# Kernel tuning notes

Measured on AMD Instinct MI355X. Metric: run time of the kernel, lower is better.

## Reference

```python
import jax, jax.numpy as jnp
import numpy as np

N_NODES = 100000
D = 128          # out_channels
H = 128          # hidden_dim
N_EDGES = 1000000


def setup_inputs() -> dict:
    key = jax.random.key(0)
    k_z, k_e, k_w1, k_b1, k_w2, k_b2 = jax.random.split(key, 6)
    z = jax.random.normal(k_z, (N_NODES, D), dtype=jnp.float32)
    edge_label_index = jax.random.randint(k_e, (2, N_EDGES), 0, N_NODES, dtype=jnp.int64)
    # nn.Linear default init: U(-1/sqrt(fan_in), 1/sqrt(fan_in))
    lim1 = 1.0 / np.sqrt(2 * D)
    lim2 = 1.0 / np.sqrt(H)
    W1 = jax.random.uniform(k_w1, (2 * D, H), jnp.float32, -lim1, lim1)
    b1 = jax.random.uniform(k_b1, (H,), jnp.float32, -lim1, lim1)
    W2 = jax.random.uniform(k_w2, (H, 1), jnp.float32, -lim2, lim2)
    b2 = jax.random.uniform(k_b2, (1,), jnp.float32, -lim2, lim2)
    return {"z": z, "edge_label_index": edge_label_index,
            "W1": W1, "b1": b1, "W2": W2, "b2": b2}


def reference(z, edge_label_index, W1, b1, W2, b2):
    src = edge_label_index[0]
    dst = edge_label_index[1]
    # gather + concat -> [n_edges, 2D]
    edge_feat = jnp.concatenate([z[src], z[dst]], axis=-1)
    h = jax.nn.relu(edge_feat @ W1 + b1)        # [n_edges, H]
    out = (h @ W2 + b2).squeeze(-1)             # [n_edges]
    return out
```

## Files before the change

kernel.cpp:

```cpp
#include <hip/hip_runtime.h>
#include <hip/hip_fp16.h>

typedef _Float16 half_t;
typedef __attribute__((ext_vector_type(2))) _Float16 f16x2;
typedef __attribute__((ext_vector_type(8))) _Float16 f16x8;
typedef __attribute__((ext_vector_type(4))) float f32x4;


__global__ void prep_kernel(const float* __restrict__ z,
                            const float* __restrict__ W1,
                            half_t* __restrict__ zh,
                            half_t* __restrict__ w1s, int n8) {
    if (blockIdx.x < 128) {
        const int t = blockIdx.x * 256 + threadIdx.x;
        const int j  = t & 7;
        const int L  = (t >> 3) & 63;
        const int nt = (t >> 9) & 15;
        const int ks = t >> 13;
        const int k    = ks * 32 + (L >> 4) * 8 + j;
        const int ncol = nt * 16 + (L & 15);
        const int row  = (ncol < 128) ? k : 128 + k;
        w1s[t] = (half_t)W1[row * 128 + (ncol & 127)];
    } else {
        const int t = (blockIdx.x - 128) * 256 + threadIdx.x;
        if (t < n8) {
            const float4 a = reinterpret_cast<const float4*>(z)[2 * t];
            const float4 b = reinterpret_cast<const float4*>(z)[2 * t + 1];
            f16x8 o;
            o[0] = (_Float16)a.x; o[1] = (_Float16)a.y;
            o[2] = (_Float16)a.z; o[3] = (_Float16)a.w;
            o[4] = (_Float16)b.x; o[5] = (_Float16)b.y;
            o[6] = (_Float16)b.z; o[7] = (_Float16)b.w;
            reinterpret_cast<f16x8*>(zh)[t] = o;
        }
    }
}

__global__ __launch_bounds__(256, 2)
void gemm_uv_kernel(const half_t* __restrict__ zh,
                    const half_t* __restrict__ w1s,
                    half_t* __restrict__ Y,
                    int n_groups, int stride_groups) {
    __shared__ __align__(16) half_t w1_lds[32768];
    const int wave = threadIdx.x >> 6;
    const int lane = threadIdx.x & 63;

#pragma unroll
    for (int rnd = 0; rnd < 16; ++rnd) {
        const int chunk = rnd * 4 + wave;
        const char* gp = (const char*)w1s + chunk * 1024 + lane * 16;
        __builtin_amdgcn_global_load_lds(
            (const __attribute__((address_space(1))) void*)gp,
            (__attribute__((address_space(3))) void*)
                ((char*)w1_lds + chunk * 1024),
            16, 0, 0);
    }
    __syncthreads();

    const int nlo  = lane & 15;
    const int quad = lane >> 4;
    const f16x8* blds = reinterpret_cast<const f16x8*>(w1_lds);

    int g = blockIdx.x * 4 + wave;
    if (g >= n_groups) return;

    const half_t* arow = zh + ((size_t)(g * 16 + nlo) * 128) + quad * 8;
    f16x8 av[4];
#pragma unroll
    for (int ks = 0; ks < 4; ++ks)
        av[ks] = *reinterpret_cast<const f16x8*>(arow + ks * 32);

    for (; g < n_groups; g += stride_groups) {
        const int gn = g + stride_groups;
        const int gp = (gn < n_groups) ? gn : g;
        const half_t* arow_n = zh + ((size_t)(gp * 16 + nlo) * 128) + quad * 8;
        f16x8 avn[4];
#pragma unroll
        for (int ks = 0; ks < 4; ++ks)
            avn[ks] = *reinterpret_cast<const f16x8*>(arow_n + ks * 32);

        f32x4 acc[16];
#pragma unroll
        for (int nt = 0; nt < 16; ++nt) acc[nt] = (f32x4){0.f, 0.f, 0.f, 0.f};

#pragma unroll
        for (int ks = 0; ks < 4; ++ks) {
            const f16x8* bp = blds + ks * 1024 + lane;
#pragma unroll
            for (int nt = 0; nt < 16; ++nt)
                acc[nt] = __builtin_amdgcn_mfma_f32_16x16x32_f16(
                    av[ks], bp[nt * 64], acc[nt], 0, 0, 0);
        }

#pragma unroll
        for (int r = 0; r < 4; ++r) {
            const int nr = g * 16 + quad * 4 + r;
            f16x8 up, vp;
#pragma unroll
            for (int t = 0; t < 8; ++t) {
                up[t] = (_Float16)acc[t][r];
                vp[t] = (_Float16)acc[8 + t][r];
            }
            *reinterpret_cast<f16x8*>(Y + (size_t)nr * 256 + nlo * 8) = up;
            *reinterpret_cast<f16x8*>(Y + (size_t)nr * 256 + 128 + nlo * 8) = vp;
        }

#pragma unroll
        for (int ks = 0; ks < 4; ++ks) av[ks] = avn[ks];
    }
}

static __device__ __forceinline__ f16x2 pair2(const f16x8& v, int p) {
    f16x2 r; r[0] = v[2 * p]; r[1] = v[2 * p + 1]; return r;
}

__global__ __launch_bounds__(256, 8)
void edge_decode_kernel(const half_t* __restrict__ Y,
                        const int* __restrict__ eidx,
                        const float* __restrict__ b1,
                        const float* __restrict__ W2,
                        const float* __restrict__ b2,
                        float* __restrict__ out,
                        int n_edges, int stride_e) {
    __shared__ __align__(16) half_t b1h[128];
    __shared__ __align__(16) half_t w2h[128];
    if (threadIdx.x < 128) {
        const int i = threadIdx.x;
        const int n = (i & 7) * 16 + (i >> 3);
        b1h[i] = (half_t)b1[n];
        w2h[i] = (half_t)W2[n];
    }
    __syncthreads();

    const int lane  = threadIdx.x & 63;
    const int sl    = lane & 15;
    const int eslot = lane >> 4;
    const f16x8 bv = reinterpret_cast<const f16x8*>(b1h)[sl];
    const f16x8 wv = reinterpret_cast<const f16x8*>(w2h)[sl];
    const float b2v = b2[0];
    const f16x2 zero2 = {(_Float16)0, (_Float16)0};

    const int w = blockIdx.x * 4 + (threadIdx.x >> 6);
    int e0 = w * 4;
    if (e0 >= n_edges) return;

    int ec = e0 + eslot; if (ec >= n_edges) ec = 0;
    int s1 = eidx[ec];
    int d1 = eidx[n_edges + ec];
    f16x8 u0 = *reinterpret_cast<const f16x8*>(Y + (size_t)s1 * 256 + sl * 8);
    f16x8 v0 = *reinterpret_cast<const f16x8*>(Y + (size_t)d1 * 256 + 128 +
                                               sl * 8);
    {
        int en = e0 + stride_e + eslot;
        if (en >= n_edges) en = 0;
        s1 = eidx[en];
        d1 = eidx[n_edges + en];
    }

    for (; e0 < n_edges; e0 += stride_e) {
        const int e = e0 + eslot;
        const bool valid = (e < n_edges);

        const f16x8 u1 = *reinterpret_cast<const f16x8*>(
            Y + (size_t)s1 * 256 + sl * 8);
        const f16x8 v1 = *reinterpret_cast<const f16x8*>(
            Y + (size_t)d1 * 256 + 128 + sl * 8);

        {
            int en = e0 + 2 * stride_e + eslot;
            if (en >= n_edges) en = 0;
            s1 = eidx[en];
            d1 = eidx[n_edges + en];
        }

        float acc = 0.f;
#pragma unroll
        for (int p = 0; p < 4; ++p) {
            f16x2 h2 = pair2(u0, p) + pair2(v0, p) + pair2(bv, p);
            h2 = __builtin_elementwise_max(h2, zero2);
            acc = __builtin_amdgcn_fdot2(h2, pair2(wv, p), acc, false);
        }
        acc += __shfl_xor(acc, 1);
        acc += __shfl_xor(acc, 2);
        acc += __shfl_xor(acc, 4);
        acc += __shfl_xor(acc, 8);
        if (sl == 0 && valid) out[e] = acc + b2v;

        u0 = u1; v0 = v1;
    }
}

__global__ void naive_edge_kernel(const float* __restrict__ z,
                                  const int* __restrict__ eidx,
                                  const float* __restrict__ W1,
                                  const float* __restrict__ b1,
                                  const float* __restrict__ W2,
                                  const float* __restrict__ b2,
                                  float* __restrict__ out, int n_edges) {
    __shared__ float feat[256];
    __shared__ float red[2];
    const int e = blockIdx.x;
    const int t = threadIdx.x;
    const int s = eidx[e], d = eidx[n_edges + e];
    feat[t] = z[(size_t)s * 128 + t];
    feat[128 + t] = z[(size_t)d * 128 + t];
    __syncthreads();
    float h = b1[t];
    for (int k = 0; k < 256; ++k) h = fmaf(feat[k], W1[k * 128 + t], h);
    float p = fmaxf(h, 0.f) * W2[t];
    for (int off = 32; off; off >>= 1) p += __shfl_down(p, off);
    if ((t & 63) == 0) red[t >> 6] = p;
    __syncthreads();
    if (t == 0) out[e] = red[0] + red[1] + b2[0];
}

extern "C" void kernel_launch(void* const* d_in, const int* in_sizes, int n_in,
                              void* d_out, int out_size, void* d_ws,
                              size_t ws_size, hipStream_t stream) {
    const float* z   = (const float*)d_in[0];
    const int* eidx  = (const int*)d_in[1];
    const float* W1  = (const float*)d_in[2];
    const float* b1  = (const float*)d_in[3];
    const float* W2  = (const float*)d_in[4];
    const float* b2  = (const float*)d_in[5];
    float* out       = (float*)d_out;

    const int nz      = in_sizes[0];
    const int n_nodes = nz / 128;
    const int n_edges = in_sizes[1] / 2;

    const size_t Y_bytes   = (size_t)n_nodes * 256 * sizeof(half_t);
    const size_t zh_bytes  = (size_t)nz * sizeof(half_t);
    const size_t w1s_bytes = 32768 * sizeof(half_t);

    if (ws_size >= Y_bytes + zh_bytes + w1s_bytes) {
        half_t* Y   = (half_t*)d_ws;
        half_t* zh  = (half_t*)((char*)d_ws + Y_bytes);
        half_t* w1s = (half_t*)((char*)d_ws + Y_bytes + zh_bytes);

        const int n8 = nz / 8;
        const int zblocks = (n8 + 255) / 256;
        prep_kernel<<<128 + zblocks, 256, 0, stream>>>(z, W1, zh, w1s, n8);

        const int n_groups = n_nodes / 16;
        const int gblocks  = 512;
        gemm_uv_kernel<<<gblocks, 256, 0, stream>>>(zh, w1s, Y, n_groups,
                                                    gblocks * 4);

        const int eblocks = 2048;
        edge_decode_kernel<<<eblocks, 256, 0, stream>>>(
            Y, eidx, b1, W2, b2, out, n_edges, eblocks * 4 * 4);
    } else {
        naive_edge_kernel<<<n_edges, 128, 0, stream>>>(z, eidx, W1, b1, W2, b2,
                                                       out, n_edges);
    }
}
```

Measured before the change: 213.5 us.

## Split node GEMM output halves across block pairs to halve LDS and registers

The per-node projection GEMM now splits its 256 output columns (U and V halves) across paired blocks, with each block loading only 32 KB of W1 into LDS and keeping 8 accumulators instead of 16. The W1 swizzle in the prep kernel is reordered so each half is contiguous. Launch bounds rise to 4 blocks per CU and the grid doubles, aiming for more occupancy and better latency hiding. In exchange, every zh row is now loaded twice, once by each half-block.

```diff
diff --git a/kernel.cpp b/kernel.cpp
--- a/kernel.cpp
+++ b/kernel.cpp
@@ -13,14 +13,14 @@
                             half_t* __restrict__ w1s, int n8) {
     if (blockIdx.x < 128) {
         const int t = blockIdx.x * 256 + threadIdx.x;
-        const int j  = t & 7;
-        const int L  = (t >> 3) & 63;
-        const int nt = (t >> 9) & 15;
-        const int ks = t >> 13;
-        const int k    = ks * 32 + (L >> 4) * 8 + j;
-        const int ncol = nt * 16 + (L & 15);
-        const int row  = (ncol < 128) ? k : 128 + k;
-        w1s[t] = (half_t)W1[row * 128 + (ncol & 127)];
+        const int j    = t & 7;
+        const int L    = (t >> 3) & 63;
+        const int nt   = (t >> 9) & 7;
+        const int ks   = (t >> 12) & 3;
+        const int half = t >> 14;
+        const int k = ks * 32 + (L >> 4) * 8 + j;
+        const int c = nt * 16 + (L & 15);
+        w1s[t] = (half_t)W1[(half * 128 + k) * 128 + c];
     } else {
         const int t = (blockIdx.x - 128) * 256 + threadIdx.x;
         if (t < n8) {
@@ -36,19 +36,22 @@
     }
 }
 
-__global__ __launch_bounds__(256, 2)
+__global__ __launch_bounds__(256, 4)
 void gemm_uv_kernel(const half_t* __restrict__ zh,
                     const half_t* __restrict__ w1s,
                     half_t* __restrict__ Y,
                     int n_groups, int stride_groups) {
-    __shared__ __align__(16) half_t w1_lds[32768];
+    __shared__ __align__(16) half_t w1_lds[16384];
     const int wave = threadIdx.x >> 6;
     const int lane = threadIdx.x & 63;
-
-#pragma unroll
-    for (int rnd = 0; rnd < 16; ++rnd) {
+    const int h    = blockIdx.x & 1;
+    const int gb   = blockIdx.x >> 1;
+
+#pragma unroll
+    for (int rnd = 0; rnd < 8; ++rnd) {
         const int chunk = rnd * 4 + wave;
-        const char* gp = (const char*)w1s + chunk * 1024 + lane * 16;
+        const char* gp = (const char*)w1s + h * 32768 + chunk * 1024 +
+                         lane * 16;
         __builtin_amdgcn_global_load_lds(
             (const __attribute__((address_space(1))) void*)gp,
             (__attribute__((address_space(3))) void*)
@@ -61,8 +64,7 @@
     const int quad = lane >> 4;
     const f16x8* blds = reinterpret_cast<const f16x8*>(w1_lds);
 
-    int g = blockIdx.x * 4 + wave;
-    if (g >= n_groups) return;
+    int g = gb * 4 + wave;
 
     const half_t* arow = zh + ((size_t)(g * 16 + nlo) * 128) + quad * 8;
     f16x8 av[4];
@@ -72,22 +74,22 @@
 
     for (; g < n_groups; g += stride_groups) {
         const int gn = g + stride_groups;
-        const int gp = (gn < n_groups) ? gn : g;
-        const half_t* arow_n = zh + ((size_t)(gp * 16 + nlo) * 128) + quad * 8;
+        const int gpi = (gn < n_groups) ? gn : g;
+        const half_t* arow_n = zh + ((size_t)(gpi * 16 + nlo) * 128) + quad * 8;
         f16x8 avn[4];
 #pragma unroll
         for (int ks = 0; ks < 4; ++ks)
             avn[ks] = *reinterpret_cast<const f16x8*>(arow_n + ks * 32);
 
-        f32x4 acc[16];
-#pragma unroll
-        for (int nt = 0; nt < 16; ++nt) acc[nt] = (f32x4){0.f, 0.f, 0.f, 0.f};
+        f32x4 acc[8];
+#pragma unroll
+        for (int nt = 0; nt < 8; ++nt) acc[nt] = (f32x4){0.f, 0.f, 0.f, 0.f};
 
 #pragma unroll
         for (int ks = 0; ks < 4; ++ks) {
-            const f16x8* bp = blds + ks * 1024 + lane;
-#pragma unroll
-            for (int nt = 0; nt < 16; ++nt)
+            const f16x8* bp = blds + ks * 512 + lane;
+#pragma unroll
+            for (int nt = 0; nt < 8; ++nt)
                 acc[nt] = __builtin_amdgcn_mfma_f32_16x16x32_f16(
                     av[ks], bp[nt * 64], acc[nt], 0, 0, 0);
         }
@@ -95,14 +97,11 @@
 #pragma unroll
         for (int r = 0; r < 4; ++r) {
             const int nr = g * 16 + quad * 4 + r;
-            f16x8 up, vp;
-#pragma unroll
-            for (int t = 0; t < 8; ++t) {
-                up[t] = (_Float16)acc[t][r];
-                vp[t] = (_Float16)acc[8 + t][r];
-            }
-            *reinterpret_cast<f16x8*>(Y + (size_t)nr * 256 + nlo * 8) = up;
-            *reinterpret_cast<f16x8*>(Y + (size_t)nr * 256 + 128 + nlo * 8) = vp;
+            f16x8 up;
+#pragma unroll
+            for (int t = 0; t < 8; ++t) up[t] = (_Float16)acc[t][r];
+            *reinterpret_cast<f16x8*>(Y + (size_t)nr * 256 + h * 128 +
+                                      nlo * 8) = up;
         }
 
 #pragma unroll
@@ -243,9 +242,9 @@
         prep_kernel<<<128 + zblocks, 256, 0, stream>>>(z, W1, zh, w1s, n8);
 
         const int n_groups = n_nodes / 16;
-        const int gblocks  = 512;
+        const int gblocks  = 1024;
         gemm_uv_kernel<<<gblocks, 256, 0, stream>>>(zh, w1s, Y, n_groups,
-                                                    gblocks * 4);
+                                                    (gblocks / 2) * 4);
 
         const int eblocks = 2048;
         edge_decode_kernel<<<eblocks, 256, 0, stream>>>(
```

Result: slower. 225.8 us (+5.7%).
